# Kernel optimization log

Hardware: AMD Instinct MI355X
Metric: run time of the kernel (lower is better)

## Reference

```python
import jax, jax.numpy as jnp
import numpy as np

B, S, E, H = 2, 2048, 1024, 16
D = E // H
SCALE = D ** -0.5


def setup_inputs() -> dict:
    key = jax.random.key(0)
    k1, k2, k3, k4, k5 = jax.random.split(key, 5)
    x = jax.random.normal(k1, (B, S, E), dtype=jnp.float32)
    # torch Linear weights: [out, in]
    W_attn = jax.random.normal(k2, (3 * E, E), dtype=jnp.float32) * (E ** -0.5)
    b_attn = jax.random.normal(k3, (3 * E,), dtype=jnp.float32) * 0.02
    W_proj = jax.random.normal(k4, (E, E), dtype=jnp.float32) * (E ** -0.5)
    b_proj = jax.random.normal(k5, (E,), dtype=jnp.float32) * 0.02
    mask = jnp.tril(jnp.ones((S, S), dtype=jnp.int32))[None, None]  # causal [1,1,S,S]
    return {"x": x, "W_attn": W_attn, "b_attn": b_attn,
            "W_proj": W_proj, "b_proj": b_proj, "mask": mask}


def reference(x, W_attn, b_attn, W_proj, b_proj, mask):
    # fused qkv projection: [B,S,3E]
    qkv = jnp.einsum('bse,fe->bsf', x, W_attn) + b_attn
    q, k, v = jnp.split(qkv, 3, axis=-1)
    # split heads -> [B,H,S,D]
    def heads(t):
        return t.reshape(B, S, H, D).transpose(0, 2, 1, 3)
    q, k, v = heads(q), heads(k), heads(v)
    # scaled dot-product attention with causal mask
    w = jnp.einsum('bhqd,bhkd->bhqk', q, k) * SCALE
    w = jnp.where(mask == 0, jnp.finfo(w.dtype).min, w)
    w = jax.nn.softmax(w, axis=-1)  # attn dropout p=0 (eval)
    o = jnp.einsum('bhqk,bhkd->bhqd', w, v)
    # merge heads -> [B,S,E]
    o = o.transpose(0, 2, 1, 3).reshape(B, S, E)
    out = jnp.einsum('bse,fe->bsf', o, W_proj) + b_proj  # resid dropout p=0
    return out
```

## Files before the change

kernel.cpp:

```cpp
#include <hip/hip_runtime.h>
#include <hip/hip_bf16.h>

typedef unsigned short u16;
typedef unsigned int u32;
typedef float f32x4 __attribute__((ext_vector_type(4)));
typedef short bf16x8 __attribute__((ext_vector_type(8)));

#define BB 2
#define SS 2048
#define EE 1024
#define HH 16
#define DD 64
#define QSCALE 0.18033688011f

__device__ __forceinline__ u16 f2bf(float f) {
    union { u32 i; float f; } x; x.f = f;
    return (u16)((x.i + 0x7FFFu + ((x.i >> 16) & 1u)) >> 16);
}
__device__ __forceinline__ u32 pkbf(float a, float b) {
    __hip_bfloat162 h = __float22bfloat162_rn(make_float2(a, b));
    union { __hip_bfloat162 h; u32 u; } c; c.h = h; return c.u;
}

#define MFMA16(a, b, c) __builtin_amdgcn_mfma_f32_16x16x32_bf16((a), (b), (c), 0, 0, 0)

__device__ __forceinline__ void gld16(const u16* g, u16* l) {
    __builtin_amdgcn_global_load_lds(
        (const __attribute__((address_space(1))) void*)g,
        (__attribute__((address_space(3))) void*)l,
        16, 0, 0);
}

__global__ __launch_bounds__(256) void convert_all(
    const float* __restrict__ x, const float* __restrict__ wa,
    const float* __restrict__ wp, u16* __restrict__ dst)
{
    const size_t n0 = (size_t)4096 * 1024;
    const size_t n1 = n0 + (size_t)3072 * 1024;
    size_t i = ((size_t)blockIdx.x * 256 + threadIdx.x) * 4;
    const float* s;
    size_t off;
    if (i < n0)      { s = x;  off = 0;  }
    else if (i < n1) { s = wa; off = n0; }
    else             { s = wp; off = n1; }
    float4 v = *(const float4*)(s + (i - off));
    uint2 o;
    o.x = pkbf(v.x, v.y);
    o.y = pkbf(v.z, v.w);
    *(uint2*)(dst + i) = o;
}

__global__ __launch_bounds__(512, 4) void gemm_qkv(
    const u16* __restrict__ A, const u16* __restrict__ B, const float* __restrict__ bias,
    u16* __restrict__ Qo, u16* __restrict__ Ko, u16* __restrict__ Vto)
{
    __shared__ __align__(16) u16 SMEM[16384];
    u16* As = SMEM;
    u16* Bs = SMEM + 8192;
    const int n0 = blockIdx.x * 128, m0 = blockIdx.y * 128;
    const int tid = threadIdx.x;
    const int wave = tid >> 6, lane = tid & 63;
    const int l16 = lane & 15, quad = lane >> 4;
    const int wm = wave >> 2, wn = wave & 3;
    const int ldr = lane >> 3;
    const int csw = ((lane & 7) ^ ldr) * 8;

    f32x4 acc[4][2];
#pragma unroll
    for (int i = 0; i < 4; ++i)
#pragma unroll
        for (int j = 0; j < 2; ++j) acc[i][j] = f32x4{0.f, 0.f, 0.f, 0.f};

    const int aorb = wave >> 2;
    u16* stgbuf = aorb ? Bs : As;
    const u16* stgsrc = aorb ? B : A;
    const int stgbase = aorb ? n0 : m0;

    for (int k0 = 0; k0 < 1024; k0 += 64) {
        __syncthreads();
#pragma unroll
        for (int t = 0; t < 4; ++t) {
            const int c = (wave & 3) * 4 + t;
            const int row = c * 8 + ldr;
            gld16(stgsrc + (size_t)(stgbase + row) * 1024 + k0 + csw,
                  &stgbuf[c * 512 + lane * 8]);
        }
        __syncthreads();
#pragma unroll
        for (int ks = 0; ks < 2; ++ks) {
            bf16x8 af[4], bf[2];
#pragma unroll
            for (int i = 0; i < 4; ++i)
                af[i] = *(const bf16x8*)&As[(wm * 64 + i * 16 + l16) * 64 +
                                            ((ks * 4 + quad) ^ (l16 & 7)) * 8];
#pragma unroll
            for (int j = 0; j < 2; ++j)
                bf[j] = *(const bf16x8*)&Bs[(wn * 32 + j * 16 + l16) * 64 +
                                            ((ks * 4 + quad) ^ (l16 & 7)) * 8];
#pragma unroll
            for (int i = 0; i < 4; ++i)
#pragma unroll
                for (int j = 0; j < 2; ++j)
                    acc[i][j] = MFMA16(af[i], bf[j], acc[i][j]);
        }
    }

    const int part = blockIdx.x >> 3;
    const int hbase = (blockIdx.x & 7) << 1;
    if (part != 2) {
        const int h = hbase + (wn >> 1);
#pragma unroll
        for (int j = 0; j < 2; ++j) {
            const int f = n0 + wn * 32 + j * 16 + l16;
            const int d = f & 63;
            const float bj = bias[f];
#pragma unroll
            for (int i = 0; i < 4; ++i) {
#pragma unroll
                for (int r = 0; r < 4; ++r) {
                    const int m = m0 + wm * 64 + i * 16 + quad * 4 + r;
                    const int b = m >> 11, s = m & 2047;
                    const float val = acc[i][j][r] + bj;
                    if (part == 0)
                        Qo[(((size_t)(b * HH + h)) * SS + s) * DD + d] = f2bf(val * QSCALE);
                    else
                        Ko[(((size_t)(b * HH + h)) * SS + s) * DD + d] = f2bf(val);
                }
            }
        }
    } else {
        u16* T = SMEM;
#pragma unroll
        for (int wmr = 0; wmr < 2; ++wmr) {
            __syncthreads();
            if (wm == wmr) {
#pragma unroll
                for (int j = 0; j < 2; ++j) {
                    const float bj = bias[n0 + wn * 32 + j * 16 + l16];
#pragma unroll
                    for (int i = 0; i < 4; ++i) {
                        uint2 pw;
                        pw.x = pkbf(acc[i][j][0] + bj, acc[i][j][1] + bj);
                        pw.y = pkbf(acc[i][j][2] + bj, acc[i][j][3] + bj);
                        *(uint2*)&T[(wn * 32 + j * 16 + l16) * 72 + i * 16 + quad * 4] = pw;
                    }
                }
            }
            __syncthreads();
            const int frow = tid >> 2;
            const int qtr = tid & 3;
            const int h = hbase + (frow >> 6);
            const int d = frow & 63;
            const int mg = m0 + wmr * 64;
            const int b = mg >> 11, sbase = mg & 2047;
            u16* dstrow = Vto + (((size_t)(b * HH + h)) * DD + d) * SS + sbase;
#pragma unroll
            for (int l = 0; l < 4; ++l) {
                const int mo = qtr * 16 + l * 4;
                *(uint2*)(dstrow + mo) = *(const uint2*)&T[frow * 72 + mo];
            }
        }
    }
}

__global__ __launch_bounds__(512, 4) void gemm_proj(
    const u16* __restrict__ A, const u16* __restrict__ B, const float* __restrict__ bias,
    float* __restrict__ out)
{
    __shared__ __align__(16) u16 SMEM[12288];
    u16* As = SMEM;
    u16* Bs = SMEM + 4096;
    const int n0 = blockIdx.x * 128, m0 = blockIdx.y * 64;
    const int tid = threadIdx.x;
    const int wave = tid >> 6, lane = tid & 63;
    const int l16 = lane & 15, quad = lane >> 4;
    const int wm = wave >> 2, wn = wave & 3;
    const int ldr = lane >> 3;
    const int csw = ((lane & 7) ^ ldr) * 8;

    f32x4 acc[2][2];
#pragma unroll
    for (int i = 0; i < 2; ++i)
#pragma unroll
        for (int j = 0; j < 2; ++j) acc[i][j] = f32x4{0.f, 0.f, 0.f, 0.f};

    for (int k0 = 0; k0 < 1024; k0 += 64) {
        __syncthreads();
#pragma unroll
        for (int t = 0; t < 3; ++t) {
            const int c = wave * 3 + t;
            if (c < 8) {
                const int row = c * 8 + ldr;
                gld16(A + (size_t)(m0 + row) * 1024 + k0 + csw, &As[c * 512 + lane * 8]);
            } else {
                const int c2 = c - 8;
                const int row = c2 * 8 + ldr;
                gld16(B + (size_t)(n0 + row) * 1024 + k0 + csw, &Bs[c2 * 512 + lane * 8]);
            }
        }
        __syncthreads();
#pragma unroll
        for (int ks = 0; ks < 2; ++ks) {
            bf16x8 af[2], bf[2];
#pragma unroll
            for (int i = 0; i < 2; ++i)
                af[i] = *(const bf16x8*)&As[(wm * 32 + i * 16 + l16) * 64 +
                                            ((ks * 4 + quad) ^ (l16 & 7)) * 8];
#pragma unroll
            for (int j = 0; j < 2; ++j)
                bf[j] = *(const bf16x8*)&Bs[(wn * 32 + j * 16 + l16) * 64 +
                                            ((ks * 4 + quad) ^ (l16 & 7)) * 8];
#pragma unroll
            for (int i = 0; i < 2; ++i)
#pragma unroll
                for (int j = 0; j < 2; ++j)
                    acc[i][j] = MFMA16(af[i], bf[j], acc[i][j]);
        }
    }
#pragma unroll
    for (int j = 0; j < 2; ++j) {
        const int f = n0 + wn * 32 + j * 16 + l16;
        const float bj = bias[f];
#pragma unroll
        for (int i = 0; i < 2; ++i) {
#pragma unroll
            for (int r = 0; r < 4; ++r) {
                const int m = m0 + wm * 32 + i * 16 + quad * 4 + r;
                out[(size_t)m * EE + f] = acc[i][j][r] + bj;
            }
        }
    }
}

__global__ __launch_bounds__(256, 4) void attn(
    const u16* __restrict__ Q, const u16* __restrict__ K, const u16* __restrict__ VT,
    u16* __restrict__ O)
{
    const int qb = 31 - (int)blockIdx.x;
    const int bh = blockIdx.y;
    const int tid = threadIdx.x;
    const int wave = tid >> 6, lane = tid & 63;
    const int l16 = lane & 15, quad = lane >> 4;
    const int ldr = lane >> 3;
    const int csw = ((lane & 7) ^ ldr) * 8;
    __shared__ __align__(16) u16 Ks[64 * 64];
    __shared__ __align__(16) u16 Vts[64 * 64];
    __shared__ __align__(16) u16 Ps[64 * 72];

    const u16* qptr = Q + (size_t)bh * SS * DD;
    const u16* kptr = K + (size_t)bh * SS * DD;
    const u16* vtptr = VT + (size_t)bh * DD * SS;

    const int qrow = qb * 64 + wave * 16 + l16;
    bf16x8 bq[2];
#pragma unroll
    for (int ks = 0; ks < 2; ++ks)
        bq[ks] = *(const bf16x8*)(qptr + (size_t)qrow * DD + ks * 32 + quad * 8);

    float lp = 0.f;
    f32x4 o_acc[4];
#pragma unroll
    for (int j = 0; j < 4; ++j) o_acc[j] = f32x4{0.f, 0.f, 0.f, 0.f};

    for (int kb = 0; kb <= qb; ++kb) {
        const int k0 = kb * 64;
        __syncthreads();
#pragma unroll
        for (int t = 0; t < 2; ++t) {
            const int a0 = wave * 2 + t;
            const int row = a0 * 8 + ldr;
            gld16(kptr + (size_t)(k0 + row) * DD + csw, &Ks[a0 * 512 + lane * 8]);
            gld16(vtptr + (size_t)row * SS + k0 + csw, &Vts[a0 * 512 + lane * 8]);
        }
        __syncthreads();

        f32x4 s[4];
#pragma unroll
        for (int j = 0; j < 4; ++j) s[j] = f32x4{0.f, 0.f, 0.f, 0.f};
#pragma unroll
        for (int ks = 0; ks < 2; ++ks) {
#pragma unroll
            for (int j = 0; j < 4; ++j) {
                bf16x8 ak = *(const bf16x8*)&Ks[(j * 16 + l16) * 64 +
                                                ((ks * 4 + quad) ^ (l16 & 7)) * 8];
                s[j] = MFMA16(ak, bq[ks], s[j]);
            }
        }

        if (kb == qb) {
#pragma unroll
            for (int j = 0; j < 4; ++j)
#pragma unroll
                for (int r = 0; r < 4; ++r) {
                    const int key = k0 + j * 16 + quad * 4 + r;
                    if (key > qrow) s[j][r] = -INFINITY;
                }
        }
#pragma unroll
        for (int j = 0; j < 4; ++j) {
            const float p0 = __builtin_amdgcn_exp2f(s[j][0]);
            const float p1 = __builtin_amdgcn_exp2f(s[j][1]);
            const float p2 = __builtin_amdgcn_exp2f(s[j][2]);
            const float p3 = __builtin_amdgcn_exp2f(s[j][3]);
            lp += (p0 + p1) + (p2 + p3);
            uint2 pw; pw.x = pkbf(p0, p1); pw.y = pkbf(p2, p3);
            *(uint2*)&Ps[(wave * 16 + l16) * 72 + j * 16 + quad * 4] = pw;
        }

#pragma unroll
        for (int ks = 0; ks < 2; ++ks) {
            bf16x8 bp = *(const bf16x8*)&Ps[(wave * 16 + l16) * 72 + ks * 32 + quad * 8];
#pragma unroll
            for (int j = 0; j < 4; ++j) {
                bf16x8 av = *(const bf16x8*)&Vts[(j * 16 + l16) * 64 +
                                                 ((ks * 4 + quad) ^ (l16 & 7)) * 8];
                o_acc[j] = MFMA16(av, bp, o_acc[j]);
            }
        }
    }

    const int b = bh >> 4, h = bh & 15;
    float l = lp;
    l += __shfl_xor(l, 16);
    l += __shfl_xor(l, 32);
    const float inv = 1.0f / l;
#pragma unroll
    for (int j = 0; j < 4; ++j) {
        uint2 o4;
        o4.x = pkbf(o_acc[j][0] * inv, o_acc[j][1] * inv);
        o4.y = pkbf(o_acc[j][2] * inv, o_acc[j][3] * inv);
        *(uint2*)&O[((size_t)(b * SS + qrow)) * EE + h * DD + j * 16 + quad * 4] = o4;
    }
}

extern "C" void kernel_launch(void* const* d_in, const int* in_sizes, int n_in,
                              void* d_out, int out_size, void* d_ws, size_t ws_size,
                              hipStream_t stream) {
    const float* x      = (const float*)d_in[0];
    const float* W_attn = (const float*)d_in[1];
    const float* b_attn = (const float*)d_in[2];
    const float* W_proj = (const float*)d_in[3];
    const float* b_proj = (const float*)d_in[4];
    float* out = (float*)d_out;

    u16* xb  = (u16*)d_ws;
    u16* wab = xb + (size_t)4096 * 1024;
    u16* wpb = wab + (size_t)3072 * 1024;
    u16* qw  = wpb + (size_t)1024 * 1024;
    u16* kw  = qw + (size_t)BB * HH * SS * DD;
    u16* vtw = kw + (size_t)BB * HH * SS * DD;
    u16* ow  = xb;

    convert_all<<<8192, 256, 0, stream>>>(x, W_attn, W_proj, xb);
    gemm_qkv<<<dim3(24, 32), 512, 0, stream>>>(xb, wab, b_attn, qw, kw, vtw);
    attn<<<dim3(32, 32), 256, 0, stream>>>(qw, kw, vtw, ow);
    gemm_proj<<<dim3(8, 64), 512, 0, stream>>>(ow, wpb, b_proj, out);
}
```

Before: 197.2 us.

## Pair causal query blocks per attention CTA and double-buffer K/V tiles

```diff
diff --git a/kernel.cpp b/kernel.cpp
--- a/kernel.cpp
+++ b/kernel.cpp
@@ -232,104 +232,121 @@
     }
 }
 
-__global__ __launch_bounds__(256, 4) void attn(
+__global__ __launch_bounds__(256, 2) void attn(
     const u16* __restrict__ Q, const u16* __restrict__ K, const u16* __restrict__ VT,
     u16* __restrict__ O)
 {
-    const int qb = 31 - (int)blockIdx.x;
+    const int p = blockIdx.x;
     const int bh = blockIdx.y;
     const int tid = threadIdx.x;
     const int wave = tid >> 6, lane = tid & 63;
     const int l16 = lane & 15, quad = lane >> 4;
     const int ldr = lane >> 3;
     const int csw = ((lane & 7) ^ ldr) * 8;
-    __shared__ __align__(16) u16 Ks[64 * 64];
-    __shared__ __align__(16) u16 Vts[64 * 64];
+    __shared__ __align__(16) u16 Ks[2][64 * 64];
+    __shared__ __align__(16) u16 Vts[2][64 * 64];
     __shared__ __align__(16) u16 Ps[64 * 72];
 
     const u16* qptr = Q + (size_t)bh * SS * DD;
     const u16* kptr = K + (size_t)bh * SS * DD;
     const u16* vtptr = VT + (size_t)bh * DD * SS;
-
-    const int qrow = qb * 64 + wave * 16 + l16;
-    bf16x8 bq[2];
-#pragma unroll
-    for (int ks = 0; ks < 2; ++ks)
-        bq[ks] = *(const bf16x8*)(qptr + (size_t)qrow * DD + ks * 32 + quad * 8);
-
-    float lp = 0.f;
-    f32x4 o_acc[4];
-#pragma unroll
-    for (int j = 0; j < 4; ++j) o_acc[j] = f32x4{0.f, 0.f, 0.f, 0.f};
-
-    for (int kb = 0; kb <= qb; ++kb) {
-        const int k0 = kb * 64;
+    const int b = bh >> 4, h = bh & 15;
+
+    for (int half = 0; half < 2; ++half) {
+        const int qb = half ? p : 31 - p;
+        const int qrow = qb * 64 + wave * 16 + l16;
+        bf16x8 bq[2];
+#pragma unroll
+        for (int ks = 0; ks < 2; ++ks)
+            bq[ks] = *(const bf16x8*)(qptr + (size_t)qrow * DD + ks * 32 + quad * 8);
+
+        float lp = 0.f;
+        f32x4 o_acc[4];
+#pragma unroll
+        for (int j = 0; j < 4; ++j) o_acc[j] = f32x4{0.f, 0.f, 0.f, 0.f};
+
         __syncthreads();
 #pragma unroll
         for (int t = 0; t < 2; ++t) {
             const int a0 = wave * 2 + t;
             const int row = a0 * 8 + ldr;
-            gld16(kptr + (size_t)(k0 + row) * DD + csw, &Ks[a0 * 512 + lane * 8]);
-            gld16(vtptr + (size_t)row * SS + k0 + csw, &Vts[a0 * 512 + lane * 8]);
-        }
-        __syncthreads();
-
-        f32x4 s[4];
-#pragma unroll
-        for (int j = 0; j < 4; ++j) s[j] = f32x4{0.f, 0.f, 0.f, 0.f};
-#pragma unroll
-        for (int ks = 0; ks < 2; ++ks) {
+            gld16(kptr + (size_t)row * DD + csw, &Ks[0][a0 * 512 + lane * 8]);
+            gld16(vtptr + (size_t)row * SS + csw, &Vts[0][a0 * 512 + lane * 8]);
+        }
+
+        for (int kb = 0; kb <= qb; ++kb) {
+            const int cur = kb & 1;
+            const int k0 = kb * 64;
+            __syncthreads();
+            if (kb < qb) {
+                const int kn = k0 + 64;
+#pragma unroll
+                for (int t = 0; t < 2; ++t) {
+                    const int a0 = wave * 2 + t;
+                    const int row = a0 * 8 + ldr;
+                    gld16(kptr + (size_t)(kn + row) * DD + csw,
+                          &Ks[cur ^ 1][a0 * 512 + lane * 8]);
+                    gld16(vtptr + (size_t)row * SS + kn + csw,
+                          &Vts[cur ^ 1][a0 * 512 + lane * 8]);
+                }
+            }
+
+            f32x4 s[4];
+#pragma unroll
+            for (int j = 0; j < 4; ++j) s[j] = f32x4{0.f, 0.f, 0.f, 0.f};
+#pragma unroll
+            for (int ks = 0; ks < 2; ++ks) {
+#pragma unroll
+                for (int j = 0; j < 4; ++j) {
+                    bf16x8 ak = *(const bf16x8*)&Ks[cur][(j * 16 + l16) * 64 +
+                                                    ((ks * 4 + quad) ^ (l16 & 7)) * 8];
+                    s[j] = MFMA16(ak, bq[ks], s[j]);
+                }
+            }
+
+            if (kb == qb) {
+#pragma unroll
+                for (int j = 0; j < 4; ++j)
+#pragma unroll
+                    for (int r = 0; r < 4; ++r) {
+                        const int key = k0 + j * 16 + quad * 4 + r;
+                        if (key > qrow) s[j][r] = -INFINITY;
+                    }
+            }
 #pragma unroll
             for (int j = 0; j < 4; ++j) {
-                bf16x8 ak = *(const bf16x8*)&Ks[(j * 16 + l16) * 64 +
-                                                ((ks * 4 + quad) ^ (l16 & 7)) * 8];
-                s[j] = MFMA16(ak, bq[ks], s[j]);
-            }
-        }
-
-        if (kb == qb) {
-#pragma unroll
-            for (int j = 0; j < 4; ++j)
-#pragma unroll
-                for (int r = 0; r < 4; ++r) {
-                    const int key = k0 + j * 16 + quad * 4 + r;
-                    if (key > qrow) s[j][r] = -INFINITY;
-                }
-        }
+                const float p0 = __builtin_amdgcn_exp2f(s[j][0]);
+                const float p1 = __builtin_amdgcn_exp2f(s[j][1]);
+                const float p2 = __builtin_amdgcn_exp2f(s[j][2]);
+                const float p3 = __builtin_amdgcn_exp2f(s[j][3]);
+                lp += (p0 + p1) + (p2 + p3);
+                uint2 pw; pw.x = pkbf(p0, p1); pw.y = pkbf(p2, p3);
+                *(uint2*)&Ps[(wave * 16 + l16) * 72 + j * 16 + quad * 4] = pw;
+            }
+
+#pragma unroll
+            for (int ks = 0; ks < 2; ++ks) {
+                bf16x8 bp = *(const bf16x8*)&Ps[(wave * 16 + l16) * 72 + ks * 32 + quad * 8];
+#pragma unroll
+                for (int j = 0; j < 4; ++j) {
+                    bf16x8 av = *(const bf16x8*)&Vts[cur][(j * 16 + l16) * 64 +
+                                                    ((ks * 4 + quad) ^ (l16 & 7)) * 8];
+                    o_acc[j] = MFMA16(av, bp, o_acc[j]);
+                }
+            }
+        }
+
+        float l = lp;
+        l += __shfl_xor(l, 16);
+        l += __shfl_xor(l, 32);
+        const float inv = 1.0f / l;
 #pragma unroll
         for (int j = 0; j < 4; ++j) {
-            const float p0 = __builtin_amdgcn_exp2f(s[j][0]);
-            const float p1 = __builtin_amdgcn_exp2f(s[j][1]);
-            const float p2 = __builtin_amdgcn_exp2f(s[j][2]);
-            const float p3 = __builtin_amdgcn_exp2f(s[j][3]);
-            lp += (p0 + p1) + (p2 + p3);
-            uint2 pw; pw.x = pkbf(p0, p1); pw.y = pkbf(p2, p3);
-            *(uint2*)&Ps[(wave * 16 + l16) * 72 + j * 16 + quad * 4] = pw;
-        }
-
-#pragma unroll
-        for (int ks = 0; ks < 2; ++ks) {
-            bf16x8 bp = *(const bf16x8*)&Ps[(wave * 16 + l16) * 72 + ks * 32 + quad * 8];
-#pragma unroll
-            for (int j = 0; j < 4; ++j) {
-                bf16x8 av = *(const bf16x8*)&Vts[(j * 16 + l16) * 64 +
-                                                 ((ks * 4 + quad) ^ (l16 & 7)) * 8];
-                o_acc[j] = MFMA16(av, bp, o_acc[j]);
-            }
-        }
-    }
-
-    const int b = bh >> 4, h = bh & 15;
-    float l = lp;
-    l += __shfl_xor(l, 16);
-    l += __shfl_xor(l, 32);
-    const float inv = 1.0f / l;
-#pragma unroll
-    for (int j = 0; j < 4; ++j) {
-        uint2 o4;
-        o4.x = pkbf(o_acc[j][0] * inv, o_acc[j][1] * inv);
-        o4.y = pkbf(o_acc[j][2] * inv, o_acc[j][3] * inv);
-        *(uint2*)&O[((size_t)(b * SS + qrow)) * EE + h * DD + j * 16 + quad * 4] = o4;
+            uint2 o4;
+            o4.x = pkbf(o_acc[j][0] * inv, o_acc[j][1] * inv);
+            o4.y = pkbf(o_acc[j][2] * inv, o_acc[j][3] * inv);
+            *(uint2*)&O[((size_t)(b * SS + qrow)) * EE + h * DD + j * 16 + quad * 4] = o4;
+        }
     }
 }
 
@@ -353,6 +370,6 @@
 
     convert_all<<<8192, 256, 0, stream>>>(x, W_attn, W_proj, xb);
     gemm_qkv<<<dim3(24, 32), 512, 0, stream>>>(xb, wab, b_attn, qw, kw, vtw);
-    attn<<<dim3(32, 32), 256, 0, stream>>>(qw, kw, vtw, ow);
+    attn<<<dim3(16, 32), 256, 0, stream>>>(qw, kw, vtw, ow);
     gemm_proj<<<dim3(8, 64), 512, 0, stream>>>(ow, wpb, b_proj, out);
 }
```

After: 188.2 us. 1.05x faster.
